# Kernel optimization log

Hardware: AMD Instinct MI355X
Metric: run time of the kernel (lower is better)

## Reference

```python
import jax, jax.numpy as jnp
from jax import lax
import numpy as np

DIM = 48
HEADS = 2
HIDDEN = 96  # int(dim * 2.0)
EPS_LN = 1e-5
EPS_NORM = 1e-12


def _ln(x, w, b):
    # WithBias LayerNorm over channel dim (dim=1 in NCHW == last dim in b,(hw),c)
    mu = jnp.mean(x, axis=1, keepdims=True)
    var = jnp.var(x, axis=1, keepdims=True)
    return (x - mu) / jnp.sqrt(var + EPS_LN) * w[None, :, None, None] + b[None, :, None, None]


def _conv1x1(x, w, b):
    # w: [O, C, 1, 1]
    return jnp.einsum('bchw,oc->bohw', x, w[:, :, 0, 0]) + b[None, :, None, None]


def _dwconv3(x, w, b):
    # w: [C, 1, 3, 3], groups=C
    y = lax.conv_general_dilated(x, w, (1, 1), 'SAME',
                                 feature_group_count=x.shape[1],
                                 dimension_numbers=('NCHW', 'OIHW', 'NCHW'))
    return y + b[None, :, None, None]


def _l2norm(x):
    n = jnp.sqrt(jnp.sum(x * x, axis=-1, keepdims=True))
    return x / jnp.maximum(n, EPS_NORM)


def setup_inputs() -> dict:
    key = jax.random.key(0)
    ks = jax.random.split(key, 12)
    s = 0.02
    inp = {
        'x': jax.random.normal(ks[0], (2, DIM, 64, 64), jnp.float32),
        'norm1_w': jnp.ones((DIM,), jnp.float32),
        'norm1_b': jnp.zeros((DIM,), jnp.float32),
        'qkv_w': jax.random.normal(ks[1], (DIM * 3, DIM, 1, 1), jnp.float32) * s,
        'qkv_b': jnp.zeros((DIM * 3,), jnp.float32),
        'qkvdw_w': jax.random.normal(ks[2], (DIM * 3, 1, 3, 3), jnp.float32) * s,
        'qkvdw_b': jnp.zeros((DIM * 3,), jnp.float32),
        'temperature': jnp.ones((HEADS, 1, 1), jnp.float32),
        'proj_w': jax.random.normal(ks[3], (DIM, DIM, 1, 1), jnp.float32) * s,
        'proj_b': jnp.zeros((DIM,), jnp.float32),
        'norm2_w': jnp.ones((DIM,), jnp.float32),
        'norm2_b': jnp.zeros((DIM,), jnp.float32),
        'fi_w': jax.random.normal(ks[4], (HIDDEN * 2, DIM, 1, 1), jnp.float32) * s,
        'fi_b': jnp.zeros((HIDDEN * 2,), jnp.float32),
        'fdw_w': jax.random.normal(ks[5], (HIDDEN * 2, 1, 3, 3), jnp.float32) * s,
        'fdw_b': jnp.zeros((HIDDEN * 2,), jnp.float32),
        'fo_w': jax.random.normal(ks[6], (DIM, HIDDEN, 1, 1), jnp.float32) * s,
        'fo_b': jnp.zeros((DIM,), jnp.float32),
    }
    return inp


def _block(x, norm1_w, norm1_b, qkv_w, qkv_b, qkvdw_w, qkvdw_b, temperature,
           proj_w, proj_b, norm2_w, norm2_b, fi_w, fi_b, fdw_w, fdw_b, fo_w, fo_b):
    b, c, h, w = x.shape
    n = h * w
    chead = c // HEADS
    # --- attention branch ---
    xn = _ln(x, norm1_w, norm1_b)
    qkv = _dwconv3(_conv1x1(xn, qkv_w, qkv_b), qkvdw_w, qkvdw_b)
    q, k, v = jnp.split(qkv, 3, axis=1)
    def to_heads(t):  # [b, heads*chead, h, w] -> [b, heads, n, chead]
        return t.reshape(b, HEADS, chead, n).transpose(0, 1, 3, 2)
    q, k, v = to_heads(q), to_heads(k), to_heads(v)
    q = _l2norm(q)
    k = _l2norm(k)
    attn = jnp.einsum('bhnc,bhmc->bhnm', q, k) * temperature[None]
    attn = jax.nn.softmax(attn, axis=-1)
    out = jnp.einsum('bhnm,bhmc->bhnc', attn, v)
    out = out.transpose(0, 1, 3, 2).reshape(b, c, h, w)
    x = x + _conv1x1(out, proj_w, proj_b)
    # --- ffn branch ---
    xn = _ln(x, norm2_w, norm2_b)
    y = _dwconv3(_conv1x1(xn, fi_w, fi_b), fdw_w, fdw_b)
    y1, y2 = jnp.split(y, 2, axis=1)
    y = jax.nn.gelu(y1, approximate=False) * y2
    x = x + _conv1x1(y, fo_w, fo_b)
    return x


def reference(x, norm1_w, norm1_b, qkv_w, qkv_b, qkvdw_w, qkvdw_b, temperature,
              proj_w, proj_b, norm2_w, norm2_b, fi_w, fi_b, fdw_w, fdw_b, fo_w, fo_b):
    return _block(x, norm1_w, norm1_b, qkv_w, qkv_b, qkvdw_w, qkvdw_b, temperature,
                  proj_w, proj_b, norm2_w, norm2_b, fi_w, fi_b, fdw_w, fdw_b, fo_w, fo_b)
```

## Files before the change

kernel.cpp:

```cpp
#include <hip/hip_runtime.h>
#include <hip/hip_bf16.h>
#include <math.h>

#define NPIX 4096
#define DIMC 48
#define NB 2
#define SPLIT 4

typedef __attribute__((ext_vector_type(8))) short short8;
typedef __attribute__((ext_vector_type(4))) short short4s;
typedef __attribute__((ext_vector_type(4))) float floatx4;

static __device__ inline short f2bf(float f) {
    union { float f; unsigned u; } v; v.f = f;
    unsigned r = (v.u + 0x7FFFu + ((v.u >> 16) & 1u)) >> 16;
    return (short)r;
}
static __device__ inline float bf2f(short s) {
    union { unsigned u; float f; } v;
    v.u = ((unsigned)(unsigned short)s) << 16;
    return v.f;
}

__global__ void k_prepw(const float* __restrict__ qkvw, const float* __restrict__ fiw,
                        const float* __restrict__ fow, const float* __restrict__ projw,
                        short* __restrict__ qkvwbf, short* __restrict__ fiwbf,
                        short* __restrict__ fowbf, short* __restrict__ projwbf) {
    int idx = blockIdx.x * 256 + threadIdx.x;
    if (idx < 144 * 64) {
        int o = idx >> 6, c = idx & 63;
        qkvwbf[idx] = (c < 48) ? f2bf(qkvw[o * 48 + c]) : (short)0;
        return;
    }
    idx -= 144 * 64;
    if (idx < 192 * 64) {
        int o = idx >> 6, c = idx & 63;
        fiwbf[idx] = (c < 48) ? f2bf(fiw[o * 48 + c]) : (short)0;
        return;
    }
    idx -= 192 * 64;
    if (idx < 48 * 96) {
        fowbf[idx] = f2bf(fow[idx]);
        return;
    }
    idx -= 48 * 96;
    if (idx < 48 * 64) {
        int o = idx >> 6, c = idx & 63;
        projwbf[idx] = (c < 48) ? f2bf(projw[o * 48 + c]) : (short)0;
    }
}

__global__ __launch_bounds__(256) void k_ln_conv_mfma(
    const float* __restrict__ xin, const float* __restrict__ lw, const float* __restrict__ lb,
    const short* __restrict__ wbf, const float* __restrict__ cb,
    short* __restrict__ outbf, int OC)
{
    int px0 = blockIdx.x * 32;
    int b = blockIdx.y;
    int t = threadIdx.x;
    int w = t >> 6, lane = t & 63, l15 = lane & 15, quad = lane >> 4;

    __shared__ float psum[8][32], psq[8][32];
    __shared__ float muS[32], rsS[32];
    __shared__ short xnbf[32][72];

    int px = t & 31, g = t >> 5;
    *(unsigned*)&xnbf[px][48 + g * 2] = 0u;

    float v[6];
    float s = 0.f, sq = 0.f;
#pragma unroll
    for (int i = 0; i < 6; i++) {
        v[i] = xin[((size_t)b * 48 + g * 6 + i) * (size_t)NPIX + px0 + px];
        s += v[i]; sq += v[i] * v[i];
    }
    psum[g][px] = s; psq[g][px] = sq;
    __syncthreads();
    if (t < 32) {
        float ss = 0.f, qq = 0.f;
#pragma unroll
        for (int i = 0; i < 8; i++) { ss += psum[i][t]; qq += psq[i][t]; }
        float mu = ss * (1.f / 48.f);
        float var = qq * (1.f / 48.f) - mu * mu;
        muS[t] = mu; rsS[t] = rsqrtf(var + 1e-5f);
    }
    __syncthreads();
    {
        float mu = muS[px], rs = rsS[px];
#pragma unroll
        for (int i = 0; i < 6; i++) {
            int c = g * 6 + i;
            xnbf[px][c] = f2bf((v[i] - mu) * rs * lw[c] + lb[c]);
        }
    }
    __syncthreads();
    floatx4 zf = {0.f, 0.f, 0.f, 0.f};
    int oct = OC >> 4;
    int njobs = 2 * oct;
    for (int job = w; job < njobs; job += 4) {
        int pt = job / oct, ot = job % oct;
        short8 a0 = *(const short8*)&xnbf[pt * 16 + l15][quad * 8];
        short8 a1 = *(const short8*)&xnbf[pt * 16 + l15][32 + quad * 8];
        const short* wb = wbf + (ot * 16 + l15) * 64;
        short8 b0 = *(const short8*)(wb + quad * 8);
        short8 b1 = *(const short8*)(wb + 32 + quad * 8);
        floatx4 c = __builtin_amdgcn_mfma_f32_16x16x32_bf16(a0, b0, zf, 0, 0, 0);
        c = __builtin_amdgcn_mfma_f32_16x16x32_bf16(a1, b1, c, 0, 0, 0);
        int oc = ot * 16 + l15;
        float bi = cb[oc];
        short4s st;
#pragma unroll
        for (int r = 0; r < 4; r++) st[r] = f2bf(c[r] + bi);
        *(short4s*)(outbf + ((size_t)b * OC + oc) * (size_t)NPIX + px0 + pt * 16 + quad * 4) = st;
    }
}

__global__ __launch_bounds__(256) void k_dw3heads(
    const short* __restrict__ qkv_pre, const float* __restrict__ dww,
    const float* __restrict__ dwb, const float* __restrict__ temp,
    short* __restrict__ Qbf, short* __restrict__ Kbf, short* __restrict__ Vbf)
{
    int px0 = blockIdx.x * 16;
    int y = blockIdx.y, b = blockIdx.z;
    int t = threadIdx.x;
    int wx0 = px0 - 8; if (wx0 < 0) wx0 = 0; if (wx0 > 32) wx0 = 32;
    int xoff = px0 - wx0;

    __shared__ short stage[3][144][40];
    __shared__ float q2[16][148];

    for (int seg = t; seg < 3 * 144 * 4; seg += 256) {
        int q = seg & 3, idx = seg >> 2;
        int c = idx % 144, r = idx / 144;
        int yy = y + r - 1;
        short8 ld = {};
        if ((unsigned)yy < 64u)
            ld = *(const short8*)(qkv_pre + (size_t)(b * 144 + c) * NPIX + yy * 64 + wx0 + q * 8);
        *(short8*)&stage[r][c][q * 8] = ld;
    }
    __syncthreads();
    int px = t & 15, g = t >> 4;
    {
        int sbase = xoff + px;
        for (int i = 0; i < 9; i++) {
            int c = g * 9 + i;
            const float* wp = dww + c * 9;
            float acc = dwb[c];
#pragma unroll
            for (int dy = 0; dy < 3; dy++) {
#pragma unroll
                for (int dx = -1; dx <= 1; dx++) {
                    int si = sbase + dx;
                    if ((unsigned)si < 32u)
                        acc += bf2f(stage[dy][c][si]) * wp[dy * 3 + dx + 1];
                }
            }
            q2[px][c] = acc;
        }
    }
    __syncthreads();
    if (t < 32) {
        int hpx = t & 15, h = t >> 4;
        int n = y * 64 + px0 + hpx;
        int bh = b * 2 + h;
        float q[24], k[24], vv[24]; float sqs = 0.f, sks = 0.f;
#pragma unroll
        for (int c = 0; c < 24; c++) {
            q[c] = q2[hpx][h * 24 + c];       sqs += q[c] * q[c];
            k[c] = q2[hpx][48 + h * 24 + c];  sks += k[c] * k[c];
            vv[c] = q2[hpx][96 + h * 24 + c];
        }
        float rq = temp[h] / fmaxf(sqrtf(sqs), 1e-12f);
        float rk = 1.f / fmaxf(sqrtf(sks), 1e-12f);
        short qs[32], ks[32];
#pragma unroll
        for (int c = 0; c < 24; c++) { qs[c] = f2bf(q[c] * rq); ks[c] = f2bf(k[c] * rk); }
#pragma unroll
        for (int c = 24; c < 32; c++) { qs[c] = 0; ks[c] = 0; }
        size_t ro = ((size_t)bh * NPIX + n) * 32;
#pragma unroll
        for (int i = 0; i < 4; i++) {
            short8 a, bb;
#pragma unroll
            for (int j = 0; j < 8; j++) { a[j] = qs[i * 8 + j]; bb[j] = ks[i * 8 + j]; }
            *(short8*)(Qbf + ro + i * 8) = a;
            *(short8*)(Kbf + ro + i * 8) = bb;
        }
        int r5 = n & 31;
        int vcol = (n & ~31) + ((r5 & 15) * 2 + (r5 >> 4));
#pragma unroll
        for (int c = 0; c < 24; c++)
            Vbf[((size_t)bh * 32 + c) * NPIX + vcol] = f2bf(vv[c]);
#pragma unroll
        for (int c = 24; c < 32; c++)
            Vbf[((size_t)bh * 32 + c) * NPIX + vcol] = 0;
    }
}

__global__ __launch_bounds__(256) void k_attn_mfma(const short* __restrict__ Qbf,
                                                   const short* __restrict__ Kbf,
                                                   const short* __restrict__ Vbf,
                                                   float* __restrict__ Opart,
                                                   float* __restrict__ lpart) {
    int qt = blockIdx.x, s = blockIdx.y, bh = blockIdx.z;
    int t = threadIdx.x;
    int w = t >> 6, lane = t & 63, l15 = lane & 15, quad = lane >> 4;

    __shared__ short tileK[2][32][40];
    __shared__ short tileV[2][32][40];
    __shared__ short P[4][16][40];

    int qrow0 = qt * 64 + w * 16;
    short8 aq = *(const short8*)(Qbf + ((size_t)bh * NPIX + qrow0 + l15) * 32 + quad * 8);

    int i = t & 127;
    int rr = i >> 2, qh = i & 3;
    bool isV = t >= 128;
    const short* srcK = Kbf + ((size_t)bh * NPIX + rr) * 32 + qh * 8;
    const short* srcV = Vbf + ((size_t)(bh * 32 + rr)) * NPIX + qh * 8;
    int dstoff = rr * 40 + qh * 8;

    int key0 = s * (NPIX / SPLIT);
    {
        short8 ld = isV ? *(const short8*)(srcV + key0)
                        : *(const short8*)(srcK + (size_t)key0 * 32);
        short* dst = (isV ? &tileV[0][0][0] : &tileK[0][0][0]) + dstoff;
        *(short8*)dst = ld;
    }

    floatx4 zf = {0.f, 0.f, 0.f, 0.f};
    floatx4 o0 = zf, o1 = zf;
    float ls[4] = {0.f, 0.f, 0.f, 0.f};

    const int NKT = (NPIX / SPLIT) / 32;
    for (int kt = 0; kt < NKT; kt++) {
        __syncthreads();
        int cur = kt & 1;
        short8 ld = {};
        if (kt < NKT - 1) {
            int kabs = key0 + (kt + 1) * 32;
            ld = isV ? *(const short8*)(srcV + kabs)
                     : *(const short8*)(srcK + (size_t)kabs * 32);
        }
        short8 b0  = *(const short8*)&tileK[cur][l15][quad * 8];
        short8 b1  = *(const short8*)&tileK[cur][l15 + 16][quad * 8];
        short8 vb0 = *(const short8*)&tileV[cur][l15][quad * 8];
        short8 vb1 = *(const short8*)&tileV[cur][l15 + 16][quad * 8];
        floatx4 s0 = __builtin_amdgcn_mfma_f32_16x16x32_bf16(aq, b0, zf, 0, 0, 0);
        floatx4 s1 = __builtin_amdgcn_mfma_f32_16x16x32_bf16(aq, b1, zf, 0, 0, 0);
#pragma unroll
        for (int r = 0; r < 4; r++) {
            float p0 = __expf(s0[r]);
            float p1 = __expf(s1[r]);
            ls[r] += p0 + p1;
            __hip_bfloat162 pk = __float22bfloat162_rn(make_float2(p0, p1));
            *(unsigned*)&P[w][quad * 4 + r][l15 * 2] = *(unsigned*)&pk;
        }
        short8 ap = *(const short8*)&P[w][l15][quad * 8];
        o0 = __builtin_amdgcn_mfma_f32_16x16x32_bf16(ap, vb0, o0, 0, 0, 0);
        o1 = __builtin_amdgcn_mfma_f32_16x16x32_bf16(ap, vb1, o1, 0, 0, 0);
        if (kt < NKT - 1) {
            short* dst = (isV ? &tileV[1 - cur][0][0] : &tileK[1 - cur][0][0]) + dstoff;
            *(short8*)dst = ld;
        }
    }
#pragma unroll
    for (int m = 1; m < 16; m <<= 1) {
#pragma unroll
        for (int r = 0; r < 4; r++) ls[r] += __shfl_xor(ls[r], m, 64);
    }
#pragma unroll
    for (int r = 0; r < 4; r++) {
        int n = qrow0 + quad * 4 + r;
        size_t base2 = (size_t)(bh * SPLIT + s) * 32;
        Opart[(base2 + l15) * NPIX + n] = o0[r];
        Opart[(base2 + 16 + l15) * NPIX + n] = o1[r];
        if (l15 == 0) lpart[((size_t)(bh * SPLIT + s)) * NPIX + n] = ls[r];
    }
}

__global__ __launch_bounds__(256) void k_projred(
    const float* __restrict__ x, const float* __restrict__ Opart,
    const float* __restrict__ lpart, const short* __restrict__ projwbf,
    const float* __restrict__ bias, float* __restrict__ x1)
{
    int px0 = blockIdx.x * 32;
    int b = blockIdx.y;
    int t = threadIdx.x;
    int w = t >> 6, lane = t & 63, l15 = lane & 15, quad = lane >> 4;

    __shared__ __align__(16) short Ash[32][72];
    __shared__ float rlsh[2][32];

    if (t < 64) {
        int h = t >> 5, px = t & 31;
        float l = 0.f;
#pragma unroll
        for (int s = 0; s < SPLIT; s++)
            l += lpart[((size_t)((b * 2 + h) * SPLIT + s)) * NPIX + px0 + px];
        rlsh[h][px] = 1.f / l;
    }
    {
        int px = t & 31, j = t >> 5;
        *(unsigned*)&Ash[px][48 + j * 2] = 0u;
    }
    __syncthreads();
#pragma unroll
    for (int pi = 0; pi < 6; pi++) {
        int idx = pi * 256 + t;
        int px = idx & 31, c = idx >> 5;
        int h = c / 24, ch = c % 24;
        float acc = 0.f;
#pragma unroll
        for (int s = 0; s < SPLIT; s++)
            acc += Opart[(((size_t)((b * 2 + h) * SPLIT + s)) * 32 + ch) * NPIX + px0 + px];
        Ash[px][c] = f2bf(acc * rlsh[h][px]);
    }
    __syncthreads();
    floatx4 zf = {0.f, 0.f, 0.f, 0.f};
    for (int job = w; job < 6; job += 4) {
        int pt = job / 3, ot = job % 3;
        short8 a0 = *(const short8*)&Ash[pt * 16 + l15][quad * 8];
        short8 a1 = *(const short8*)&Ash[pt * 16 + l15][32 + quad * 8];
        const short* wb = projwbf + (ot * 16 + l15) * 64;
        short8 b0 = *(const short8*)(wb + quad * 8);
        short8 b1 = *(const short8*)(wb + 32 + quad * 8);
        floatx4 c = __builtin_amdgcn_mfma_f32_16x16x32_bf16(a0, b0, zf, 0, 0, 0);
        c = __builtin_amdgcn_mfma_f32_16x16x32_bf16(a1, b1, c, 0, 0, 0);
        int oc = ot * 16 + l15;
        float bi = bias[oc];
#pragma unroll
        for (int r = 0; r < 4; r++) {
            int n = px0 + pt * 16 + quad * 4 + r;
            size_t idx = ((size_t)b * 48 + oc) * NPIX + n;
            x1[idx] = x[idx] + c[r] + bi;
        }
    }
}

__global__ __launch_bounds__(256) void k_dwgatefo(
    const short* __restrict__ fp_pre, const float* __restrict__ fdww,
    const float* __restrict__ fdwb, const short* __restrict__ fowbf,
    const float* __restrict__ fob, const float* __restrict__ x1,
    float* __restrict__ out)
{
    int px0 = blockIdx.x * 16;
    int y = blockIdx.y, b = blockIdx.z;
    int t = threadIdx.x;
    int w = t >> 6, lane = t & 63, l15 = lane & 15, quad = lane >> 4;
    int wx0 = px0 - 8; if (wx0 < 0) wx0 = 0; if (wx0 > 32) wx0 = 32;
    int xoff = px0 - wx0;

    __shared__ short stage[3][192][40];
    __shared__ short yv[16][104];

    for (int seg = t; seg < 3 * 192 * 4; seg += 256) {
        int q = seg & 3, idx = seg >> 2;
        int c = idx % 192, r = idx / 192;
        int yy = y + r - 1;
        short8 ld = {};
        if ((unsigned)yy < 64u)
            ld = *(const short8*)(fp_pre + (size_t)(b * 192 + c) * NPIX + yy * 64 + wx0 + q * 8);
        *(short8*)&stage[r][c][q * 8] = ld;
    }
    __syncthreads();
    int px = t & 15, g = t >> 4;
    {
        int sbase = xoff + px;
        for (int i = 0; i < 6; i++) {
            int c = g * 6 + i;
            const float* wp  = fdww + c * 9;
            const float* wp2 = fdww + (c + 96) * 9;
            float a  = fdwb[c];
            float g2 = fdwb[c + 96];
#pragma unroll
            for (int dy = 0; dy < 3; dy++) {
#pragma unroll
                for (int dx = -1; dx <= 1; dx++) {
                    int si = sbase + dx;
                    if ((unsigned)si < 32u) {
                        a  += bf2f(stage[dy][c][si])      * wp[dy * 3 + dx + 1];
                        g2 += bf2f(stage[dy][c + 96][si]) * wp2[dy * 3 + dx + 1];
                    }
                }
            }
            float ge = 0.5f * a * (1.f + erff(a * 0.70710678118654752f));
            yv[px][c] = f2bf(ge * g2);
        }
    }
    __syncthreads();
    if (w < 3) {
        floatx4 c = {0.f, 0.f, 0.f, 0.f};
#pragma unroll
        for (int k = 0; k < 3; k++) {
            short8 a = *(const short8*)&yv[l15][k * 32 + quad * 8];
            short8 bb = *(const short8*)(fowbf + (w * 16 + l15) * 96 + k * 32 + quad * 8);
            c = __builtin_amdgcn_mfma_f32_16x16x32_bf16(a, bb, c, 0, 0, 0);
        }
        int oc = w * 16 + l15;
        float bi = fob[oc];
#pragma unroll
        for (int r = 0; r < 4; r++) {
            int n = y * 64 + px0 + quad * 4 + r;
            size_t idx = ((size_t)b * 48 + oc) * NPIX + n;
            out[idx] = x1[idx] + c[r] + bi;
        }
    }
}

extern "C" void kernel_launch(void* const* d_in, const int* in_sizes, int n_in,
                              void* d_out, int out_size, void* d_ws, size_t ws_size,
                              hipStream_t stream) {
    const float* x       = (const float*)d_in[0];
    const float* n1w     = (const float*)d_in[1];
    const float* n1b     = (const float*)d_in[2];
    const float* qkv_w   = (const float*)d_in[3];
    const float* qkv_b   = (const float*)d_in[4];
    const float* qkvdw_w = (const float*)d_in[5];
    const float* qkvdw_b = (const float*)d_in[6];
    const float* temp    = (const float*)d_in[7];
    const float* proj_w  = (const float*)d_in[8];
    const float* proj_b  = (const float*)d_in[9];
    const float* n2w     = (const float*)d_in[10];
    const float* n2b     = (const float*)d_in[11];
    const float* fi_w    = (const float*)d_in[12];
    const float* fi_b    = (const float*)d_in[13];
    const float* fdw_w   = (const float*)d_in[14];
    const float* fdw_b   = (const float*)d_in[15];
    const float* fo_w    = (const float*)d_in[16];
    const float* fo_b    = (const float*)d_in[17];

    float* ws = (float*)d_ws;
    short* qkv_pre = (short*)ws;
    short* fp_pre  = (short*)(ws + 589824);
    short* Qbf     = (short*)(ws + 1376256);
    short* Kbf     = (short*)(ws + 1638400);
    short* Vbf     = (short*)(ws + 1900544);
    float* Opart   = ws + 2162688;
    float* lpart   = ws + 4259840;
    float* x1      = ws + 4325376;
    short* qkvwbf  = (short*)(ws + 4718592);
    short* fiwbf   = qkvwbf + 9216;
    short* fowbf   = fiwbf + 12288;
    short* projwbf = fowbf + 4608;

    {
        int total = 144 * 64 + 192 * 64 + 48 * 96 + 48 * 64;
        k_prepw<<<(total + 255) / 256, 256, 0, stream>>>(qkv_w, fi_w, fo_w, proj_w,
                                                         qkvwbf, fiwbf, fowbf, projwbf);
    }
    {
        dim3 g(128, NB);
        k_ln_conv_mfma<<<g, 256, 0, stream>>>(x, n1w, n1b, qkvwbf, qkv_b, qkv_pre, 144);
    }
    {
        dim3 g(4, 64, NB);
        k_dw3heads<<<g, 256, 0, stream>>>(qkv_pre, qkvdw_w, qkvdw_b, temp, Qbf, Kbf, Vbf);
    }
    {
        dim3 g(64, SPLIT, 4);
        k_attn_mfma<<<g, 256, 0, stream>>>(Qbf, Kbf, Vbf, Opart, lpart);
    }
    {
        dim3 g(128, NB);
        k_projred<<<g, 256, 0, stream>>>(x, Opart, lpart, projwbf, proj_b, x1);
    }
    {
        dim3 g(128, NB);
        k_ln_conv_mfma<<<g, 256, 0, stream>>>(x1, n2w, n2b, fiwbf, fi_b, fp_pre, 192);
    }
    {
        dim3 g(4, 64, NB);
        k_dwgatefo<<<g, 256, 0, stream>>>(fp_pre, fdw_w, fdw_b, fowbf, fo_b, x1,
                                          (float*)d_out);
    }
}
```

Measured before the change: 151.9 us.

## Widen attention key tiles to 64 and fuse proj with LayerNorm and FFN input conv

```diff
diff --git a/kernel.cpp b/kernel.cpp
--- a/kernel.cpp
+++ b/kernel.cpp
@@ -206,62 +206,69 @@
     int t = threadIdx.x;
     int w = t >> 6, lane = t & 63, l15 = lane & 15, quad = lane >> 4;
 
-    __shared__ short tileK[2][32][40];
-    __shared__ short tileV[2][32][40];
-    __shared__ short P[4][16][40];
+    __shared__ short tileK[2][64][40];
+    __shared__ short tileV[2][32][72];
+    __shared__ short P[4][16][72];
 
     int qrow0 = qt * 64 + w * 16;
     short8 aq = *(const short8*)(Qbf + ((size_t)bh * NPIX + qrow0 + l15) * 32 + quad * 8);
 
-    int i = t & 127;
-    int rr = i >> 2, qh = i & 3;
-    bool isV = t >= 128;
-    const short* srcK = Kbf + ((size_t)bh * NPIX + rr) * 32 + qh * 8;
-    const short* srcV = Vbf + ((size_t)(bh * 32 + rr)) * NPIX + qh * 8;
-    int dstoff = rr * 40 + qh * 8;
+    int krow = t >> 2, kseg = t & 3;
+    int vch = t >> 3, vseg = t & 7;
+    const short* srcK = Kbf + ((size_t)bh * NPIX + krow) * 32 + kseg * 8;
+    const short* srcV = Vbf + ((size_t)(bh * 32 + vch)) * NPIX + vseg * 8;
 
     int key0 = s * (NPIX / SPLIT);
-    {
-        short8 ld = isV ? *(const short8*)(srcV + key0)
-                        : *(const short8*)(srcK + (size_t)key0 * 32);
-        short* dst = (isV ? &tileV[0][0][0] : &tileK[0][0][0]) + dstoff;
-        *(short8*)dst = ld;
-    }
+    *(short8*)&tileK[0][krow][kseg * 8] = *(const short8*)(srcK + (size_t)key0 * 32);
+    *(short8*)&tileV[0][vch][vseg * 8]  = *(const short8*)(srcV + key0);
 
     floatx4 zf = {0.f, 0.f, 0.f, 0.f};
     floatx4 o0 = zf, o1 = zf;
     float ls[4] = {0.f, 0.f, 0.f, 0.f};
 
-    const int NKT = (NPIX / SPLIT) / 32;
+    const int NKT = (NPIX / SPLIT) / 64;
     for (int kt = 0; kt < NKT; kt++) {
         __syncthreads();
         int cur = kt & 1;
-        short8 ld = {};
+        short8 ldK = {}, ldV = {};
         if (kt < NKT - 1) {
-            int kabs = key0 + (kt + 1) * 32;
-            ld = isV ? *(const short8*)(srcV + kabs)
-                     : *(const short8*)(srcK + (size_t)kabs * 32);
-        }
-        short8 b0  = *(const short8*)&tileK[cur][l15][quad * 8];
-        short8 b1  = *(const short8*)&tileK[cur][l15 + 16][quad * 8];
-        short8 vb0 = *(const short8*)&tileV[cur][l15][quad * 8];
-        short8 vb1 = *(const short8*)&tileV[cur][l15 + 16][quad * 8];
-        floatx4 s0 = __builtin_amdgcn_mfma_f32_16x16x32_bf16(aq, b0, zf, 0, 0, 0);
-        floatx4 s1 = __builtin_amdgcn_mfma_f32_16x16x32_bf16(aq, b1, zf, 0, 0, 0);
+            int kabs = key0 + (kt + 1) * 64;
+            ldK = *(const short8*)(srcK + (size_t)kabs * 32);
+            ldV = *(const short8*)(srcV + kabs);
+        }
+        short8 kb0 = *(const short8*)&tileK[cur][l15][quad * 8];
+        short8 kb1 = *(const short8*)&tileK[cur][16 + l15][quad * 8];
+        short8 kb2 = *(const short8*)&tileK[cur][32 + l15][quad * 8];
+        short8 kb3 = *(const short8*)&tileK[cur][48 + l15][quad * 8];
+        floatx4 s0 = __builtin_amdgcn_mfma_f32_16x16x32_bf16(aq, kb0, zf, 0, 0, 0);
+        floatx4 s1 = __builtin_amdgcn_mfma_f32_16x16x32_bf16(aq, kb1, zf, 0, 0, 0);
+        floatx4 s2 = __builtin_amdgcn_mfma_f32_16x16x32_bf16(aq, kb2, zf, 0, 0, 0);
+        floatx4 s3 = __builtin_amdgcn_mfma_f32_16x16x32_bf16(aq, kb3, zf, 0, 0, 0);
 #pragma unroll
         for (int r = 0; r < 4; r++) {
             float p0 = __expf(s0[r]);
             float p1 = __expf(s1[r]);
-            ls[r] += p0 + p1;
-            __hip_bfloat162 pk = __float22bfloat162_rn(make_float2(p0, p1));
-            *(unsigned*)&P[w][quad * 4 + r][l15 * 2] = *(unsigned*)&pk;
-        }
-        short8 ap = *(const short8*)&P[w][l15][quad * 8];
-        o0 = __builtin_amdgcn_mfma_f32_16x16x32_bf16(ap, vb0, o0, 0, 0, 0);
-        o1 = __builtin_amdgcn_mfma_f32_16x16x32_bf16(ap, vb1, o1, 0, 0, 0);
+            float p2 = __expf(s2[r]);
+            float p3 = __expf(s3[r]);
+            ls[r] += (p0 + p1) + (p2 + p3);
+            __hip_bfloat162 pk01 = __float22bfloat162_rn(make_float2(p0, p1));
+            __hip_bfloat162 pk23 = __float22bfloat162_rn(make_float2(p2, p3));
+            *(unsigned*)&P[w][quad * 4 + r][l15 * 2]      = *(unsigned*)&pk01;
+            *(unsigned*)&P[w][quad * 4 + r][32 + l15 * 2] = *(unsigned*)&pk23;
+        }
+        short8 ap0 = *(const short8*)&P[w][l15][quad * 8];
+        short8 ap1 = *(const short8*)&P[w][l15][32 + quad * 8];
+        short8 vb00 = *(const short8*)&tileV[cur][l15][quad * 8];
+        short8 vb01 = *(const short8*)&tileV[cur][l15][32 + quad * 8];
+        short8 vb10 = *(const short8*)&tileV[cur][16 + l15][quad * 8];
+        short8 vb11 = *(const short8*)&tileV[cur][16 + l15][32 + quad * 8];
+        o0 = __builtin_amdgcn_mfma_f32_16x16x32_bf16(ap0, vb00, o0, 0, 0, 0);
+        o0 = __builtin_amdgcn_mfma_f32_16x16x32_bf16(ap1, vb01, o0, 0, 0, 0);
+        o1 = __builtin_amdgcn_mfma_f32_16x16x32_bf16(ap0, vb10, o1, 0, 0, 0);
+        o1 = __builtin_amdgcn_mfma_f32_16x16x32_bf16(ap1, vb11, o1, 0, 0, 0);
         if (kt < NKT - 1) {
-            short* dst = (isV ? &tileV[1 - cur][0][0] : &tileK[1 - cur][0][0]) + dstoff;
-            *(short8*)dst = ld;
+            *(short8*)&tileK[1 - cur][krow][kseg * 8] = ldK;
+            *(short8*)&tileV[1 - cur][vch][vseg * 8]  = ldV;
         }
     }
 #pragma unroll
@@ -279,10 +286,13 @@
     }
 }
 
-__global__ __launch_bounds__(256) void k_projred(
+__global__ __launch_bounds__(256) void k_projlnfi(
     const float* __restrict__ x, const float* __restrict__ Opart,
     const float* __restrict__ lpart, const short* __restrict__ projwbf,
-    const float* __restrict__ bias, float* __restrict__ x1)
+    const float* __restrict__ projb,
+    const float* __restrict__ n2w, const float* __restrict__ n2b,
+    const short* __restrict__ fiwbf, const float* __restrict__ fib,
+    float* __restrict__ x1, short* __restrict__ fp_pre)
 {
     int px0 = blockIdx.x * 32;
     int b = blockIdx.y;
@@ -291,6 +301,10 @@
 
     __shared__ __align__(16) short Ash[32][72];
     __shared__ float rlsh[2][32];
+    __shared__ float x1sh[32][53];
+    __shared__ float psum[8][32], psq[8][32];
+    __shared__ float muS[32], rsS[32];
+    __shared__ short xnbf[32][72];
 
     if (t < 64) {
         int h = t >> 5, px = t & 31;
@@ -303,6 +317,7 @@
     {
         int px = t & 31, j = t >> 5;
         *(unsigned*)&Ash[px][48 + j * 2] = 0u;
+        *(unsigned*)&xnbf[px][48 + j * 2] = 0u;
     }
     __syncthreads();
 #pragma unroll
@@ -328,13 +343,60 @@
         floatx4 c = __builtin_amdgcn_mfma_f32_16x16x32_bf16(a0, b0, zf, 0, 0, 0);
         c = __builtin_amdgcn_mfma_f32_16x16x32_bf16(a1, b1, c, 0, 0, 0);
         int oc = ot * 16 + l15;
-        float bi = bias[oc];
+        float bi = projb[oc];
 #pragma unroll
         for (int r = 0; r < 4; r++) {
-            int n = px0 + pt * 16 + quad * 4 + r;
-            size_t idx = ((size_t)b * 48 + oc) * NPIX + n;
-            x1[idx] = x[idx] + c[r] + bi;
-        }
+            int px = pt * 16 + quad * 4 + r;
+            size_t idx = ((size_t)b * 48 + oc) * NPIX + px0 + px;
+            float val = x[idx] + c[r] + bi;
+            x1[idx] = val;
+            x1sh[px][oc] = val;
+        }
+    }
+    __syncthreads();
+    int px = t & 31, g = t >> 5;
+    float v[6];
+    float s = 0.f, sq = 0.f;
+#pragma unroll
+    for (int i = 0; i < 6; i++) {
+        v[i] = x1sh[px][g * 6 + i];
+        s += v[i]; sq += v[i] * v[i];
+    }
+    psum[g][px] = s; psq[g][px] = sq;
+    __syncthreads();
+    if (t < 32) {
+        float ss = 0.f, qq = 0.f;
+#pragma unroll
+        for (int i = 0; i < 8; i++) { ss += psum[i][t]; qq += psq[i][t]; }
+        float mu = ss * (1.f / 48.f);
+        float var = qq * (1.f / 48.f) - mu * mu;
+        muS[t] = mu; rsS[t] = rsqrtf(var + 1e-5f);
+    }
+    __syncthreads();
+    {
+        float mu = muS[px], rs = rsS[px];
+#pragma unroll
+        for (int i = 0; i < 6; i++) {
+            int c = g * 6 + i;
+            xnbf[px][c] = f2bf((v[i] - mu) * rs * n2w[c] + n2b[c]);
+        }
+    }
+    __syncthreads();
+    for (int job = w; job < 24; job += 4) {
+        int pt = job / 12, ot = job % 12;
+        short8 a0 = *(const short8*)&xnbf[pt * 16 + l15][quad * 8];
+        short8 a1 = *(const short8*)&xnbf[pt * 16 + l15][32 + quad * 8];
+        const short* wb = fiwbf + (ot * 16 + l15) * 64;
+        short8 b0 = *(const short8*)(wb + quad * 8);
+        short8 b1 = *(const short8*)(wb + 32 + quad * 8);
+        floatx4 c = __builtin_amdgcn_mfma_f32_16x16x32_bf16(a0, b0, zf, 0, 0, 0);
+        c = __builtin_amdgcn_mfma_f32_16x16x32_bf16(a1, b1, c, 0, 0, 0);
+        int oc = ot * 16 + l15;
+        float bi = fib[oc];
+        short4s st;
+#pragma unroll
+        for (int r = 0; r < 4; r++) st[r] = f2bf(c[r] + bi);
+        *(short4s*)(fp_pre + ((size_t)b * 192 + oc) * (size_t)NPIX + px0 + pt * 16 + quad * 4) = st;
     }
 }
 
@@ -463,11 +525,8 @@
     }
     {
         dim3 g(128, NB);
-        k_projred<<<g, 256, 0, stream>>>(x, Opart, lpart, projwbf, proj_b, x1);
-    }
-    {
-        dim3 g(128, NB);
-        k_ln_conv_mfma<<<g, 256, 0, stream>>>(x1, n2w, n2b, fiwbf, fi_b, fp_pre, 192);
+        k_projlnfi<<<g, 256, 0, stream>>>(x, Opart, lpart, projwbf, proj_b,
+                                          n2w, n2b, fiwbf, fi_b, x1, fp_pre);
     }
     {
         dim3 g(4, 64, NB);
```

New measurement: 150.3 us. About the same (-1.0%).
